# Kernel tuning notes

Hardware: AMD Instinct MI355X
Metric: run time of the kernel (lower is better)

The kernel has to match this reference:

```python
import jax, jax.numpy as jnp
import numpy as np

N = 131072          # batch of (action, condition) pairs
ACT_D = 12          # action_dim
COND_D = 256        # condition_dim
K = 256             # num_embeddings (codebook size)
E = 16              # embedding_dim
H1, H2 = 512, 256   # encoder_hidden_dims
COMMIT = 0.25       # commitment_cost
EPS_NORM = 1e-12    # F.normalize eps


def _normalize(x):
    n = jnp.linalg.norm(x, axis=-1, keepdims=True)
    return x / jnp.maximum(n, EPS_NORM)


def setup_inputs() -> dict:
    key = jax.random.key(0)
    ks = jax.random.split(key, 16)
    s = 0.02
    return {
        "actions": jax.random.normal(ks[0], (N, ACT_D), jnp.float32),
        "conditions": jax.random.normal(ks[1], (N, COND_D), jnp.float32),
        # encoder: (COND_D+ACT_D) -> H1 -> H2 -> E  (weights stored [in, out])
        "enc_w1": jax.random.normal(ks[2], (COND_D + ACT_D, H1), jnp.float32) * s,
        "enc_b1": jnp.zeros((H1,), jnp.float32),
        "enc_w2": jax.random.normal(ks[3], (H1, H2), jnp.float32) * s,
        "enc_b2": jnp.zeros((H2,), jnp.float32),
        "enc_w3": jax.random.normal(ks[4], (H2, E), jnp.float32) * s,
        "enc_b3": jnp.zeros((E,), jnp.float32),
        # decoder: (COND_D+E) -> H2 -> H1 -> ACT_D
        "dec_w1": jax.random.normal(ks[5], (COND_D + E, H2), jnp.float32) * s,
        "dec_b1": jnp.zeros((H2,), jnp.float32),
        "dec_w2": jax.random.normal(ks[6], (H2, H1), jnp.float32) * s,
        "dec_b2": jnp.zeros((H1,), jnp.float32),
        "dec_w3": jax.random.normal(ks[7], (H1, ACT_D), jnp.float32) * s,
        "dec_b3": jnp.zeros((ACT_D,), jnp.float32),
        # codebook, init U(-1/K, 1/K) like nn.Embedding in the module
        "embedding": jax.random.uniform(ks[8], (K, E), jnp.float32, -1.0 / K, 1.0 / K),
    }


def reference(actions, conditions, enc_w1, enc_b1, enc_w2, enc_b2, enc_w3, enc_b3,
              dec_w1, dec_b1, dec_w2, dec_b2, dec_w3, dec_b3, embedding):
    sg = jax.lax.stop_gradient
    elu = jax.nn.elu

    # ---- encoder ----
    x = jnp.concatenate([actions, conditions], axis=-1)          # [N, ACT_D+COND_D]
    h = elu(x @ enc_w1 + enc_b1)
    h = elu(h @ enc_w2 + enc_b2)
    z = h @ enc_w3 + enc_b3                                      # [N, E]

    # ---- vector quantizer (distance='cos') ----
    normed_in = sg(_normalize(z))                                # inputs.detach()
    normed_w = _normalize(embedding)
    distances = normed_in @ normed_w.T                           # [N, K] cosine sims

    idx = jnp.argmax(distances, axis=-1)                         # [N]
    quantized = embedding[idx]                                   # one-hot @ codebook == gather

    e_latent_loss = COMMIT * jnp.mean((sg(quantized) - z) ** 2)
    q_latent_loss = jnp.mean((quantized - sg(z)) ** 2)
    quantized_st = z + sg(quantized - z)                         # straight-through

    counts = jnp.zeros((K,), distances.dtype).at[idx].add(1.0)
    avg_probs = counts / N                                       # mean of one-hot encodings
    perplexity = jnp.exp(-jnp.sum(avg_probs * jnp.log(avg_probs + 1e-10)))

    # ---- contrastive loss (training branch, deterministic part) ----
    sortd = jnp.sort(distances, axis=0)                          # ascending per codeword
    n_pos = max(1, N // K)
    dis_pos = jnp.mean(sortd[-n_pos:, :], axis=0, keepdims=True) # [1, K] hardest positives
    dis_neg = sortd[: N // 2, :]                                 # [N//2, K]
    dis = jnp.concatenate([dis_pos, dis_neg], axis=0).T / 0.07   # [K, 1+N//2]
    # cross-entropy with target class 0
    contra_loss = jnp.mean(jax.nn.logsumexp(dis, axis=1) - dis[:, 0])

    # ---- decoder ----
    d = jnp.concatenate([quantized_st, conditions], axis=-1)     # [N, E+COND_D]
    d = elu(d @ dec_w1 + dec_b1)
    d = elu(d @ dec_w2 + dec_b2)
    reconstructed = d @ dec_w3 + dec_b3                          # [N, ACT_D]

    reconstruction_loss = jnp.mean((reconstructed - actions) ** 2)

    return (reconstructed, quantized_st, idx.astype(jnp.int32), q_latent_loss,
            e_latent_loss, contra_loss, perplexity, reconstruction_loss)
```

## Files before the change

### kernel.cpp

```cpp
#include <hip/hip_runtime.h>
#include <hip/hip_bf16.h>
#include <math.h>

#define NROWS 131072
#define ACT_D 12
#define COND_D 256
#define KEMB 256
#define EDIM 16
#define H1D 512
#define H2D 256
#define NB 16384

typedef __attribute__((ext_vector_type(8))) _Float16 half8;
typedef __attribute__((ext_vector_type(4))) float floatx4;
typedef unsigned short ushort_t;

#define LO_SCALE 4096.0f
#define INV_LO_SCALE 2.44140625e-4f


__global__ void init_kernel(int* counts, float* outScal) {
    int t = threadIdx.x;
    counts[t] = 0;
    if (t < 5) outScal[t] = 0.0f;
}

__device__ inline ushort_t f16bits(_Float16 h) { return __builtin_bit_cast(ushort_t, h); }
__device__ inline float f16pair(ushort_t a, ushort_t b) {
    return (float)__builtin_bit_cast(_Float16, a)
         + (float)__builtin_bit_cast(_Float16, b) * INV_LO_SCALE;
}
__device__ inline void splitf(float v, ushort_t& hi, ushort_t& lo) {
    _Float16 h = (_Float16)v;
    _Float16 l = (_Float16)((v - (float)h) * LO_SCALE);
    hi = f16bits(h); lo = f16bits(l);
}

__device__ inline void gload_lds16(const void* g, void* lds) {
    __builtin_amdgcn_global_load_lds((const __attribute__((address_space(1))) void*)g,
                                     (__attribute__((address_space(3))) void*)lds, 16, 0, 0);
}

__global__ __launch_bounds__(256)
void convw_kernel(const float* __restrict__ W, ushort_t* __restrict__ Whi,
                  ushort_t* __restrict__ Wlo, int K, int N, int Kp)
{
    int n = blockIdx.x;
    int k = blockIdx.y * 256 + threadIdx.x;
    if (k >= Kp) return;
    float v = (k < K) ? W[(long)k * N + n] : 0.0f;
    ushort_t h, l; splitf(v, h, l);
    Whi[(long)n * Kp + k] = h;
    Wlo[(long)n * Kp + k] = l;
}

template<int CONCAT>
__global__ __launch_bounds__(256, 3)
void gemm_f16x3_kernel(const void* A0v, const void* A1v,
                       const ushort_t* __restrict__ Bhi, const ushort_t* __restrict__ Blo,
                       const float* __restrict__ bias,
                       ushort_t* __restrict__ Chi, ushort_t* __restrict__ Clo,
                       int Nw, int Kp, int Kvalid)
{
    __shared__ uint lds[4096];
    const int tid = threadIdx.x;
    const int w = tid >> 6, l = tid & 63;
    const int quad = l >> 4, lr = l & 15;
    const long rowBase = (long)blockIdx.x * 64;
    const int colBase = blockIdx.y * 128;
    const int nQ = w * 32;

    floatx4 accH[4][2], accX[4][2];
#pragma unroll
    for (int i = 0; i < 4; ++i)
#pragma unroll
        for (int j = 0; j < 2; ++j) { accH[i][j] = (floatx4)(0.0f); accX[i][j] = (floatx4)(0.0f); }

    const long nIdx0 = colBase + nQ + lr;
    const ushort_t* pF0h = Bhi + nIdx0 * Kp + quad * 8;
    const ushort_t* pF1h = pF0h + 16 * Kp;
    const ushort_t* pF0l = Blo + nIdx0 * Kp + quad * 8;
    const ushort_t* pF1l = pF0l + 16 * Kp;

    uint4 bch0, bch1, bcl0, bcl1;
    auto loadB = [&](int k0) {
        bch0 = *(const uint4*)(pF0h + k0);
        bch1 = *(const uint4*)(pF1h + k0);
        bcl0 = *(const uint4*)(pF0l + k0);
        bcl1 = *(const uint4*)(pF1l + k0);
    };

    const ushort_t* pAh = (const ushort_t*)A0v + (rowBase + l) * Kp + w * 8;
    const ushort_t* pAl = (const ushort_t*)A1v + (rowBase + l) * Kp + w * 8;
    auto stageA0 = [&](int buf, int k0) {
        uint* d = &lds[buf * 2048 + w * 256];
        gload_lds16(pAh + k0, d);
        gload_lds16(pAl + k0, d + 1024);
    };

    const float* A1p = (const float*)A0v;
    const float* A2p = (const float*)A1v;
    const long grow = rowBase + l;

    auto aload = [&](float* v, int k0) {
        const int kk = k0 + w * 8;
        if (kk >= CONCAT && kk + 8 <= Kvalid) {
            const float* p = A2p + grow * COND_D + (kk - CONCAT);
            *(float4*)&v[0] = *(const float4*)p;
            *(float4*)&v[4] = *(const float4*)(p + 4);
        } else if (kk + 8 <= CONCAT) {
            const float* p = A1p + grow * CONCAT + kk;
            *(float4*)&v[0] = *(const float4*)p;
            *(float4*)&v[4] = *(const float4*)(p + 4);
        } else {
#pragma unroll
            for (int i = 0; i < 8; ++i) {
                int k = kk + i;
                v[i] = (k < CONCAT) ? A1p[grow * CONCAT + k]
                     : (k < Kvalid) ? A2p[grow * COND_D + (k - CONCAT)] : 0.0f;
            }
        }
    };
    auto awrite = [&](int buf, const float* v) {
        uint hh[4], ll[4];
#pragma unroll
        for (int i = 0; i < 4; ++i) {
            ushort_t h0, l0, h1, l1;
            splitf(v[2 * i], h0, l0);
            splitf(v[2 * i + 1], h1, l1);
            hh[i] = (uint)h0 | ((uint)h1 << 16);
            ll[i] = (uint)l0 | ((uint)l1 << 16);
        }
        *(uint4*)&lds[buf * 2048 + w * 256 + l * 4]        = *(uint4*)hh;
        *(uint4*)&lds[buf * 2048 + 1024 + w * 256 + l * 4] = *(uint4*)ll;
    };

    auto compute = [&](int buf) {
        const int base = buf * 2048;
        half8 bh0 = __builtin_bit_cast(half8, bch0);
        half8 bh1 = __builtin_bit_cast(half8, bch1);
        half8 bl0 = __builtin_bit_cast(half8, bcl0);
        half8 bl1 = __builtin_bit_cast(half8, bcl1);
#pragma unroll
        for (int im = 0; im < 4; ++im) {
            int aoff = base + quad * 256 + (im * 16 + lr) * 4;
            half8 ah = __builtin_bit_cast(half8, *(uint4*)&lds[aoff]);
            half8 al = __builtin_bit_cast(half8, *(uint4*)&lds[aoff + 1024]);
            accH[im][0] = __builtin_amdgcn_mfma_f32_16x16x32_f16(ah, bh0, accH[im][0], 0, 0, 0);
            accX[im][0] = __builtin_amdgcn_mfma_f32_16x16x32_f16(ah, bl0, accX[im][0], 0, 0, 0);
            accX[im][0] = __builtin_amdgcn_mfma_f32_16x16x32_f16(al, bh0, accX[im][0], 0, 0, 0);
            accH[im][1] = __builtin_amdgcn_mfma_f32_16x16x32_f16(ah, bh1, accH[im][1], 0, 0, 0);
            accX[im][1] = __builtin_amdgcn_mfma_f32_16x16x32_f16(ah, bl1, accX[im][1], 0, 0, 0);
            accX[im][1] = __builtin_amdgcn_mfma_f32_16x16x32_f16(al, bh1, accX[im][1], 0, 0, 0);
        }
    };

    const int kTiles = Kp / 32;
    int cur = 0;
    float v[8];

    if constexpr (CONCAT == 0) {
        stageA0(0, 0);
        loadB(0);
        __syncthreads();
    } else {
        aload(v, 0);
        loadB(0);
        awrite(0, v);
        __syncthreads();
    }

    for (int t = 0; t < kTiles; ++t) {
        const bool hasNext = (t + 1 < kTiles);
        const int k0n = (t + 1) * 32;
        if constexpr (CONCAT == 0) {
            if (hasNext) stageA0(cur ^ 1, k0n);
            compute(cur);
            if (hasNext) loadB(k0n);
        } else {
            if (hasNext) aload(v, k0n);
            compute(cur);
            if (hasNext) {
                awrite(cur ^ 1, v);
                loadB(k0n);
            }
        }
        __syncthreads();
        cur ^= 1;
    }

    float bv[2];
#pragma unroll
    for (int jn = 0; jn < 2; ++jn) bv[jn] = bias[colBase + nQ + jn * 16 + lr];
#pragma unroll
    for (int im = 0; im < 4; ++im) {
#pragma unroll
        for (int jn = 0; jn < 2; ++jn) {
            int n = colBase + nQ + jn * 16 + lr;
#pragma unroll
            for (int rr = 0; rr < 4; ++rr) {
                long m = rowBase + im * 16 + quad * 4 + rr;
                float x = accH[im][jn][rr] + accX[im][jn][rr] * INV_LO_SCALE + bv[jn];
                x = x > 0.0f ? x : (expf(x) - 1.0f);
                ushort_t h, lo; splitf(x, h, lo);
                long idx = m * Nw + n;
                Chi[idx] = h;
                Clo[idx] = lo;
            }
        }
    }
}

__global__ __launch_bounds__(256)
void quantize_kernel(const ushort_t* __restrict__ h2hi, const ushort_t* __restrict__ h2lo,
                     const float* __restrict__ W3,
                     const float* __restrict__ b3, const float* __restrict__ emb,
                     float* __restrict__ distT, float* __restrict__ outQ,
                     float* __restrict__ outIdx, int* __restrict__ counts,
                     float* __restrict__ qsum)
{
    __shared__ float h2t[16 * 260];
    __shared__ float w3t[16 * 260];
    __shared__ float nwt[256 * 20];
    __shared__ float zt[16 * 17];
    __shared__ float dt[16 * 257];
    __shared__ int   lcnt[256];
    __shared__ float swred[4];

    int t = threadIdx.x;
    long rowBase = (long)blockIdx.x * 16;

    for (int it = 0; it < 16; ++it) {
        long idx = (rowBase + it) * 256 + t;
        h2t[it * 260 + t] = f16pair(h2hi[idx], h2lo[idx]);
    }
    for (int it = 0; it < 16; ++it) {
        int flat = it * 256 + t;
        int j = flat >> 4, c = flat & 15;
        w3t[c * 260 + j] = W3[flat];
    }
    {
        float e0[16]; float ss = 0.f;
#pragma unroll
        for (int i = 0; i < 16; ++i) { e0[i] = emb[t * 16 + i]; ss += e0[i] * e0[i]; }
        float inv = 1.0f / fmaxf(sqrtf(ss), 1e-12f);
#pragma unroll
        for (int i = 0; i < 16; ++i) nwt[t * 20 + i] = e0[i] * inv;
    }
    lcnt[t] = 0;
    __syncthreads();

    int r = t >> 4, c = t & 15;
    float zacc = b3[c];
    for (int j4 = 0; j4 < 64; ++j4) {
        float4 h = *(const float4*)&h2t[r * 260 + j4 * 4];
        float4 w = *(const float4*)&w3t[c * 260 + j4 * 4];
        zacc += h.x * w.x + h.y * w.y + h.z * w.z + h.w * w.w;
    }
    float ss = zacc * zacc;
#pragma unroll
    for (int m = 1; m < 16; m <<= 1) ss += __shfl_xor(ss, m, 64);
    zt[r * 17 + c] = zacc / fmaxf(sqrtf(ss), 1e-12f);
    __syncthreads();

    float zr[16];
#pragma unroll
    for (int e = 0; e < 16; ++e) zr[e] = zt[r * 17 + e];
    float best = -1e30f; int bidx = 0;
    for (int cc = 0; cc < 16; ++cc) {
        int col = cc * 16 + c;
        float d = 0.f;
#pragma unroll
        for (int e4 = 0; e4 < 4; ++e4) {
            float4 wv = *(const float4*)&nwt[col * 20 + e4 * 4];
            d += zr[e4 * 4 + 0] * wv.x + zr[e4 * 4 + 1] * wv.y
               + zr[e4 * 4 + 2] * wv.z + zr[e4 * 4 + 3] * wv.w;
        }
        dt[r * 257 + col] = d;
        if (d > best || (d == best && col < bidx)) { best = d; bidx = col; }
    }
#pragma unroll
    for (int m = 1; m < 16; m <<= 1) {
        float ov = __shfl_xor(best, m, 64);
        int   oi = __shfl_xor(bidx, m, 64);
        if (ov > best || (ov == best && oi < bidx)) { best = ov; bidx = oi; }
    }

    float q = emb[bidx * 16 + c];
    outQ[(rowBase + r) * 16 + c] = q;
    float df = q - zacc;
    float part = df * df;
#pragma unroll
    for (int m = 1; m < 64; m <<= 1) part += __shfl_xor(part, m, 64);
    if ((t & 63) == 0) swred[t >> 6] = part;
    if (c == 0) {
        outIdx[rowBase + r] = (float)bidx;
        atomicAdd(&lcnt[bidx], 1);
    }
    __syncthreads();
    if (t == 0) atomicAdd(qsum, swred[0] + swred[1] + swred[2] + swred[3]);
    if (lcnt[t] > 0) atomicAdd(&counts[t], lcnt[t]);

    int rr = t & 15, cg = t >> 4;
    for (int i = 0; i < 16; ++i) {
        int col = i * 16 + cg;
        distT[(long)col * NROWS + rowBase + rr] = dt[rr * 257 + col];
    }
}

__global__ __launch_bounds__(1024)
void selA_kernel(const float* __restrict__ distT, int* __restrict__ stats)
{
    __shared__ int hist[NB];
    __shared__ int part[1024];
    int t = threadIdx.x, c = blockIdx.x;
    for (int i = t; i < NB; i += 1024) hist[i] = 0;
    __syncthreads();
    const float* col = distT + (long)c * NROWS;
    for (int i = t; i < NROWS; i += 1024) {
        float v = col[i];
        int b = (int)((v + 1.0f) * (NB * 0.5f));
        b = min(max(b, 0), NB - 1);
        atomicAdd(&hist[b], 1);
    }
    __syncthreads();
    const int CH = NB / 1024;
    int s = 0;
    for (int i = 0; i < CH; ++i) s += hist[t * CH + i];
    part[t] = s;
    __syncthreads();
    if (t == 0) {
        int target = NROWS / 2;
        int cum = 0; int chunk = 0;
        while (cum + part[chunk] < target) { cum += part[chunk]; ++chunk; }
        int b = chunk * CH;
        while (cum + hist[b] < target) { cum += hist[b]; ++b; }
        int medBin = b, needLow = target - cum, cntMed = hist[b];
        int cumA = 0; chunk = 1023;
        while (cumA + part[chunk] < 512) { cumA += part[chunk]; --chunk; }
        b = chunk * CH + CH - 1;
        while (cumA + hist[b] < 512) { cumA += hist[b]; --b; }
        int topBin = b, needTop = 512 - cumA, cntTop = hist[b];
        int* st = stats + c * 6;
        st[0] = medBin; st[1] = needLow; st[2] = cntMed;
        st[3] = topBin; st[4] = needTop; st[5] = cntTop;
    }
}

__global__ __launch_bounds__(1024)
void selB_kernel(const float* __restrict__ distT, const int* __restrict__ stats,
                 float* __restrict__ contra_sum)
{
    __shared__ float red[64];
    int t = threadIdx.x, c = blockIdx.x;
    const int* st = stats + c * 6;
    int medBin = st[0], needLow = st[1], cntMed = st[2];
    int topBin = st[3], needTop = st[4], cntTop = st[5];
    const float binw = 2.0f / NB;
    float mUp = -1.0f + (medBin + 1) * binw;
    const float INVT = 1.0f / 0.07f;
    const float* col = distT + (long)c * NROWS;
    float topS = 0.f, tbS = 0.f, lowS = 0.f, mbS = 0.f;
    for (int i = t; i < NROWS; i += 1024) {
        float v = col[i];
        int b = (int)((v + 1.0f) * (NB * 0.5f));
        b = min(max(b, 0), NB - 1);
        if (b > topBin)       topS += v;
        else if (b == topBin) tbS += v;
        if (b < medBin)       lowS += expf((v - mUp) * INVT);
        else if (b == medBin) mbS  += expf((v - mUp) * INVT);
    }
#pragma unroll
    for (int m = 1; m < 64; m <<= 1) {
        topS += __shfl_xor(topS, m, 64);
        tbS  += __shfl_xor(tbS, m, 64);
        lowS += __shfl_xor(lowS, m, 64);
        mbS  += __shfl_xor(mbS, m, 64);
    }
    if ((t & 63) == 0) {
        int wv = t >> 6;
        red[wv * 4 + 0] = topS; red[wv * 4 + 1] = tbS;
        red[wv * 4 + 2] = lowS; red[wv * 4 + 3] = mbS;
    }
    __syncthreads();
    if (t == 0) {
        float T0 = 0, T1 = 0, T2 = 0, T3 = 0;
        for (int wv = 0; wv < 16; ++wv) {
            T0 += red[wv * 4 + 0]; T1 += red[wv * 4 + 1];
            T2 += red[wv * 4 + 2]; T3 += red[wv * 4 + 3];
        }
        float dis_pos = (T0 + needTop * (T1 / cntTop)) * (1.0f / 512.0f);
        float S = T2 + needLow * (T3 / cntMed);
        float colContra = log1pf(S * expf((mUp - dis_pos) * INVT));
        atomicAdd(contra_sum, colContra);
    }
}

__global__ __launch_bounds__(256)
void dec3_kernel(const ushort_t* __restrict__ d2hi, const ushort_t* __restrict__ d2lo,
                 const float* __restrict__ W,
                 const float* __restrict__ bias, const float* __restrict__ actions,
                 float* __restrict__ rec, float* __restrict__ recon_sum)
{
    __shared__ float dtile[16 * 516];
    __shared__ float wt[512 * 12];
    __shared__ float red2[4];
    int t = threadIdx.x;
    long rowBase = (long)blockIdx.x * 16;
    for (int it = 0; it < 24; ++it) wt[it * 256 + t] = W[it * 256 + t];
    for (int it = 0; it < 32; ++it) {
        int flat = it * 256 + t;
        int r = flat >> 9, k = flat & 511;
        long idx = (rowBase + r) * 512 + k;
        dtile[r * 516 + k] = f16pair(d2hi[idx], d2lo[idx]);
    }
    __syncthreads();
    float part = 0.f;
    if (t < 192) {
        int r = t / 12, cc = t % 12;
        float acc = bias[cc];
        for (int k4 = 0; k4 < 128; ++k4) {
            float4 h = *(const float4*)&dtile[r * 516 + k4 * 4];
            acc += h.x * wt[(k4 * 4 + 0) * 12 + cc] + h.y * wt[(k4 * 4 + 1) * 12 + cc]
                 + h.z * wt[(k4 * 4 + 2) * 12 + cc] + h.w * wt[(k4 * 4 + 3) * 12 + cc];
        }
        rec[(rowBase + r) * 12 + cc] = acc;
        float df = acc - actions[(rowBase + r) * 12 + cc];
        part = df * df;
    }
#pragma unroll
    for (int m = 1; m < 64; m <<= 1) part += __shfl_xor(part, m, 64);
    if ((t & 63) == 0) red2[t >> 6] = part;
    __syncthreads();
    if (t == 0) atomicAdd(recon_sum, red2[0] + red2[1] + red2[2] + red2[3]);
}

__global__ void finalize_kernel(const int* __restrict__ counts, float* __restrict__ outScal)
{
    __shared__ float red[4];
    int t = threadIdx.x;
    float p = counts[t] * (1.0f / NROWS);
    float term = p * logf(p + 1e-10f);
#pragma unroll
    for (int m = 1; m < 64; m <<= 1) term += __shfl_xor(term, m, 64);
    if ((t & 63) == 0) red[t >> 6] = term;
    __syncthreads();
    if (t == 0) {
        float hsum = red[0] + red[1] + red[2] + red[3];
        float qsum = outScal[0], contra = outScal[2], recon = outScal[4];
        float ql = qsum * (1.0f / (NROWS * 16.0f));
        outScal[0] = ql;
        outScal[1] = 0.25f * ql;
        outScal[2] = contra * (1.0f / 256.0f);
        outScal[3] = expf(-hsum);
        outScal[4] = recon * (1.0f / (NROWS * 12.0f));
    }
}

extern "C" void kernel_launch(void* const* d_in, const int* in_sizes, int n_in,
                              void* d_out, int out_size, void* d_ws, size_t ws_size,
                              hipStream_t stream)
{
    const float* actions    = (const float*)d_in[0];
    const float* conditions = (const float*)d_in[1];
    const float* enc_w1 = (const float*)d_in[2];
    const float* enc_b1 = (const float*)d_in[3];
    const float* enc_w2 = (const float*)d_in[4];
    const float* enc_b2 = (const float*)d_in[5];
    const float* enc_w3 = (const float*)d_in[6];
    const float* enc_b3 = (const float*)d_in[7];
    const float* dec_w1 = (const float*)d_in[8];
    const float* dec_b1 = (const float*)d_in[9];
    const float* dec_w2 = (const float*)d_in[10];
    const float* dec_b2 = (const float*)d_in[11];
    const float* dec_w3 = (const float*)d_in[12];
    const float* dec_b3 = (const float*)d_in[13];
    const float* emb    = (const float*)d_in[14];

    float* out     = (float*)d_out;
    float* outRec  = out;
    float* outQ    = out + (long)NROWS * 12;
    float* outIdx  = out + (long)NROWS * 28;
    float* outScal = out + (long)NROWS * 29;

    ushort_t* wb    = (ushort_t*)d_out;
    ushort_t* w1hi  = wb;            ushort_t* w1lo  = wb + 147456;
    ushort_t* w2hi  = wb + 294912;   ushort_t* w2lo  = wb + 425984;
    ushort_t* wd1hi = wb + 557056;   ushort_t* wd1lo = wb + 630784;
    ushort_t* wd2hi = wb + 704512;   ushort_t* wd2lo = wb + 835584;

    float* ws = (float*)d_ws;
    int* counts = (int*)ws;
    int* stats  = (int*)(ws + 256);
    ushort_t* h2hi = (ushort_t*)(ws + 1792);
    ushort_t* h2lo = (ushort_t*)(ws + 16779008);
    ushort_t* d1hi = h2hi;
    ushort_t* d1lo = h2lo;
    float*    P1   = ws + 33556224;
    ushort_t* h1hi = (ushort_t*)P1;
    ushort_t* h1lo = (ushort_t*)(ws + 67110656);
    float*    distT = P1;
    ushort_t* d2hi = h1hi;
    ushort_t* d2lo = h1lo;

    hipLaunchKernelGGL(init_kernel, dim3(1), dim3(256), 0, stream, counts, outScal);
    hipLaunchKernelGGL(convw_kernel, dim3(512, 2), dim3(256), 0, stream, enc_w1, w1hi, w1lo, 268, 512, 288);
    hipLaunchKernelGGL(convw_kernel, dim3(256, 2), dim3(256), 0, stream, enc_w2, w2hi, w2lo, 512, 256, 512);
    hipLaunchKernelGGL(convw_kernel, dim3(256, 2), dim3(256), 0, stream, dec_w1, wd1hi, wd1lo, 272, 256, 288);
    hipLaunchKernelGGL(convw_kernel, dim3(512, 1), dim3(256), 0, stream, dec_w2, wd2hi, wd2lo, 256, 512, 256);
    hipLaunchKernelGGL((gemm_f16x3_kernel<ACT_D>), dim3(2048, 4), dim3(256), 0, stream,
                       (const void*)actions, (const void*)conditions, w1hi, w1lo, enc_b1,
                       h1hi, h1lo, H1D, 288, 268);
    hipLaunchKernelGGL((gemm_f16x3_kernel<0>), dim3(2048, 2), dim3(256), 0, stream,
                       (const void*)h1hi, (const void*)h1lo, w2hi, w2lo, enc_b2,
                       h2hi, h2lo, H2D, 512, 512);
    hipLaunchKernelGGL(quantize_kernel, dim3(8192), dim3(256), 0, stream,
                       h2hi, h2lo, enc_w3, enc_b3, emb, distT, outQ, outIdx, counts, &outScal[0]);
    hipLaunchKernelGGL(selA_kernel, dim3(256), dim3(1024), 0, stream, distT, stats);
    hipLaunchKernelGGL(selB_kernel, dim3(256), dim3(1024), 0, stream, distT, stats, &outScal[2]);
    hipLaunchKernelGGL((gemm_f16x3_kernel<EDIM>), dim3(2048, 2), dim3(256), 0, stream,
                       (const void*)outQ, (const void*)conditions, wd1hi, wd1lo, dec_b1,
                       d1hi, d1lo, H2D, 288, 272);
    hipLaunchKernelGGL((gemm_f16x3_kernel<0>), dim3(2048, 4), dim3(256), 0, stream,
                       (const void*)d1hi, (const void*)d1lo, wd2hi, wd2lo, dec_b2,
                       d2hi, d2lo, H1D, 256, 256);
    hipLaunchKernelGGL(dec3_kernel, dim3(8192), dim3(256), 0, stream,
                       d2hi, d2lo, dec_w3, dec_b3, actions, outRec, &outScal[4]);
    hipLaunchKernelGGL(finalize_kernel, dim3(1), dim3(256), 0, stream, counts, outScal);
}
```

Measured before the change: 1.470 ms.

## Drop LDS staging in split-f16 GEMM; load A fragments directly into registers with 2x2 warp tiling

The GEMM kernel no longer stages the A tile through shared memory with per-iteration barriers. Each wave now owns a 32x64 sub-tile in a 2x2 wave layout and loads its A and B MFMA fragments straight from global memory into registers, with register double-buffering. This removes the LDS traffic and __syncthreads, but A rows are now loaded redundantly by two waves and B columns by two waves. It also raises register pressure, which may hurt occupancy under the 3-blocks launch bound.

```diff
diff --git a/kernel.cpp b/kernel.cpp
--- a/kernel.cpp
+++ b/kernel.cpp
@@ -36,11 +36,6 @@
     hi = f16bits(h); lo = f16bits(l);
 }
 
-__device__ inline void gload_lds16(const void* g, void* lds) {
-    __builtin_amdgcn_global_load_lds((const __attribute__((address_space(1))) void*)g,
-                                     (__attribute__((address_space(3))) void*)lds, 16, 0, 0);
-}
-
 __global__ __launch_bounds__(256)
 void convw_kernel(const float* __restrict__ W, ushort_t* __restrict__ Whi,
                   ushort_t* __restrict__ Wlo, int K, int N, int Kp)
@@ -62,66 +57,79 @@
                        ushort_t* __restrict__ Chi, ushort_t* __restrict__ Clo,
                        int Nw, int Kp, int Kvalid)
 {
-    __shared__ uint lds[4096];
     const int tid = threadIdx.x;
     const int w = tid >> 6, l = tid & 63;
     const int quad = l >> 4, lr = l & 15;
+    const int wr = w & 1, wc = w >> 1;
     const long rowBase = (long)blockIdx.x * 64;
     const int colBase = blockIdx.y * 128;
-    const int nQ = w * 32;
-
-    floatx4 accH[4][2], accX[4][2];
-#pragma unroll
-    for (int i = 0; i < 4; ++i)
-#pragma unroll
-        for (int j = 0; j < 2; ++j) { accH[i][j] = (floatx4)(0.0f); accX[i][j] = (floatx4)(0.0f); }
-
-    const long nIdx0 = colBase + nQ + lr;
-    const ushort_t* pF0h = Bhi + nIdx0 * Kp + quad * 8;
-    const ushort_t* pF1h = pF0h + 16 * Kp;
-    const ushort_t* pF0l = Blo + nIdx0 * Kp + quad * 8;
-    const ushort_t* pF1l = pF0l + 16 * Kp;
-
-    uint4 bch0, bch1, bcl0, bcl1;
+
+    floatx4 accH[2][4], accX[2][4];
+#pragma unroll
+    for (int i = 0; i < 2; ++i)
+#pragma unroll
+        for (int j = 0; j < 4; ++j) { accH[i][j] = (floatx4)(0.0f); accX[i][j] = (floatx4)(0.0f); }
+
+    const long bcol = colBase + wc * 64 + lr;
+    const ushort_t* pB0h = Bhi + (bcol +  0) * (long)Kp + quad * 8;
+    const ushort_t* pB1h = Bhi + (bcol + 16) * (long)Kp + quad * 8;
+    const ushort_t* pB2h = Bhi + (bcol + 32) * (long)Kp + quad * 8;
+    const ushort_t* pB3h = Bhi + (bcol + 48) * (long)Kp + quad * 8;
+    const ushort_t* pB0l = Blo + (bcol +  0) * (long)Kp + quad * 8;
+    const ushort_t* pB1l = Blo + (bcol + 16) * (long)Kp + quad * 8;
+    const ushort_t* pB2l = Blo + (bcol + 32) * (long)Kp + quad * 8;
+    const ushort_t* pB3l = Blo + (bcol + 48) * (long)Kp + quad * 8;
+
+    uint4 b0h, b1h, b2h, b3h, b0l, b1l, b2l, b3l;
     auto loadB = [&](int k0) {
-        bch0 = *(const uint4*)(pF0h + k0);
-        bch1 = *(const uint4*)(pF1h + k0);
-        bcl0 = *(const uint4*)(pF0l + k0);
-        bcl1 = *(const uint4*)(pF1l + k0);
+        b0h = *(const uint4*)(pB0h + k0);
+        b1h = *(const uint4*)(pB1h + k0);
+        b2h = *(const uint4*)(pB2h + k0);
+        b3h = *(const uint4*)(pB3h + k0);
+        b0l = *(const uint4*)(pB0l + k0);
+        b1l = *(const uint4*)(pB1l + k0);
+        b2l = *(const uint4*)(pB2l + k0);
+        b3l = *(const uint4*)(pB3l + k0);
     };
 
-    const ushort_t* pAh = (const ushort_t*)A0v + (rowBase + l) * Kp + w * 8;
-    const ushort_t* pAl = (const ushort_t*)A1v + (rowBase + l) * Kp + w * 8;
-    auto stageA0 = [&](int buf, int k0) {
-        uint* d = &lds[buf * 2048 + w * 256];
-        gload_lds16(pAh + k0, d);
-        gload_lds16(pAl + k0, d + 1024);
+    const long arow0 = rowBase + wr * 32 + lr;
+    uint4 a0h, a1h, a0l, a1l;
+    uint4 n0h, n1h, n0l, n1l;
+    float v0[8], v1[8];
+
+    const ushort_t* pA0h = (const ushort_t*)A0v + arow0 * Kp + quad * 8;
+    const ushort_t* pA1h = pA0h + 16 * (long)Kp;
+    const ushort_t* pA0l = (const ushort_t*)A1v + arow0 * Kp + quad * 8;
+    const ushort_t* pA1l = pA0l + 16 * (long)Kp;
+    auto loadAnext = [&](int k0) {
+        n0h = *(const uint4*)(pA0h + k0);
+        n1h = *(const uint4*)(pA1h + k0);
+        n0l = *(const uint4*)(pA0l + k0);
+        n1l = *(const uint4*)(pA1l + k0);
     };
 
     const float* A1p = (const float*)A0v;
     const float* A2p = (const float*)A1v;
-    const long grow = rowBase + l;
-
-    auto aload = [&](float* v, int k0) {
-        const int kk = k0 + w * 8;
+    auto aloadRow = [&](float* v, long row, int k0) {
+        const int kk = k0 + quad * 8;
         if (kk >= CONCAT && kk + 8 <= Kvalid) {
-            const float* p = A2p + grow * COND_D + (kk - CONCAT);
+            const float* p = A2p + row * COND_D + (kk - CONCAT);
             *(float4*)&v[0] = *(const float4*)p;
             *(float4*)&v[4] = *(const float4*)(p + 4);
         } else if (kk + 8 <= CONCAT) {
-            const float* p = A1p + grow * CONCAT + kk;
+            const float* p = A1p + row * CONCAT + kk;
             *(float4*)&v[0] = *(const float4*)p;
             *(float4*)&v[4] = *(const float4*)(p + 4);
         } else {
 #pragma unroll
             for (int i = 0; i < 8; ++i) {
                 int k = kk + i;
-                v[i] = (k < CONCAT) ? A1p[grow * CONCAT + k]
-                     : (k < Kvalid) ? A2p[grow * COND_D + (k - CONCAT)] : 0.0f;
+                v[i] = (k < CONCAT) ? A1p[row * CONCAT + k]
+                     : (k < Kvalid) ? A2p[row * COND_D + (k - CONCAT)] : 0.0f;
             }
         }
     };
-    auto awrite = [&](int buf, const float* v) {
+    auto convertRow = [&](const float* v, uint4& h4, uint4& l4) {
         uint hh[4], ll[4];
 #pragma unroll
         for (int i = 0; i < 4; ++i) {
@@ -131,75 +139,92 @@
             hh[i] = (uint)h0 | ((uint)h1 << 16);
             ll[i] = (uint)l0 | ((uint)l1 << 16);
         }
-        *(uint4*)&lds[buf * 2048 + w * 256 + l * 4]        = *(uint4*)hh;
-        *(uint4*)&lds[buf * 2048 + 1024 + w * 256 + l * 4] = *(uint4*)ll;
+        h4 = *(uint4*)hh; l4 = *(uint4*)ll;
     };
 
-    auto compute = [&](int buf) {
-        const int base = buf * 2048;
-        half8 bh0 = __builtin_bit_cast(half8, bch0);
-        half8 bh1 = __builtin_bit_cast(half8, bch1);
-        half8 bl0 = __builtin_bit_cast(half8, bcl0);
-        half8 bl1 = __builtin_bit_cast(half8, bcl1);
-#pragma unroll
-        for (int im = 0; im < 4; ++im) {
-            int aoff = base + quad * 256 + (im * 16 + lr) * 4;
-            half8 ah = __builtin_bit_cast(half8, *(uint4*)&lds[aoff]);
-            half8 al = __builtin_bit_cast(half8, *(uint4*)&lds[aoff + 1024]);
-            accH[im][0] = __builtin_amdgcn_mfma_f32_16x16x32_f16(ah, bh0, accH[im][0], 0, 0, 0);
-            accX[im][0] = __builtin_amdgcn_mfma_f32_16x16x32_f16(ah, bl0, accX[im][0], 0, 0, 0);
-            accX[im][0] = __builtin_amdgcn_mfma_f32_16x16x32_f16(al, bh0, accX[im][0], 0, 0, 0);
-            accH[im][1] = __builtin_amdgcn_mfma_f32_16x16x32_f16(ah, bh1, accH[im][1], 0, 0, 0);
-            accX[im][1] = __builtin_amdgcn_mfma_f32_16x16x32_f16(ah, bl1, accX[im][1], 0, 0, 0);
-            accX[im][1] = __builtin_amdgcn_mfma_f32_16x16x32_f16(al, bh1, accX[im][1], 0, 0, 0);
-        }
+    auto compute = [&]() {
+        half8 A0h = __builtin_bit_cast(half8, a0h), A0l = __builtin_bit_cast(half8, a0l);
+        half8 A1h = __builtin_bit_cast(half8, a1h), A1l = __builtin_bit_cast(half8, a1l);
+        half8 B0h = __builtin_bit_cast(half8, b0h), B0l = __builtin_bit_cast(half8, b0l);
+        half8 B1h = __builtin_bit_cast(half8, b1h), B1l = __builtin_bit_cast(half8, b1l);
+        half8 B2h = __builtin_bit_cast(half8, b2h), B2l = __builtin_bit_cast(half8, b2l);
+        half8 B3h = __builtin_bit_cast(half8, b3h), B3l = __builtin_bit_cast(half8, b3l);
+        accH[0][0] = __builtin_amdgcn_mfma_f32_16x16x32_f16(A0h, B0h, accH[0][0], 0, 0, 0);
+        accX[0][0] = __builtin_amdgcn_mfma_f32_16x16x32_f16(A0h, B0l, accX[0][0], 0, 0, 0);
+        accX[0][0] = __builtin_amdgcn_mfma_f32_16x16x32_f16(A0l, B0h, accX[0][0], 0, 0, 0);
+        accH[0][1] = __builtin_amdgcn_mfma_f32_16x16x32_f16(A0h, B1h, accH[0][1], 0, 0, 0);
+        accX[0][1] = __builtin_amdgcn_mfma_f32_16x16x32_f16(A0h, B1l, accX[0][1], 0, 0, 0);
+        accX[0][1] = __builtin_amdgcn_mfma_f32_16x16x32_f16(A0l, B1h, accX[0][1], 0, 0, 0);
+        accH[0][2] = __builtin_amdgcn_mfma_f32_16x16x32_f16(A0h, B2h, accH[0][2], 0, 0, 0);
+        accX[0][2] = __builtin_amdgcn_mfma_f32_16x16x32_f16(A0h, B2l, accX[0][2], 0, 0, 0);
+        accX[0][2] = __builtin_amdgcn_mfma_f32_16x16x32_f16(A0l, B2h, accX[0][2], 0, 0, 0);
+        accH[0][3] = __builtin_amdgcn_mfma_f32_16x16x32_f16(A0h, B3h, accH[0][3], 0, 0, 0);
+        accX[0][3] = __builtin_amdgcn_mfma_f32_16x16x32_f16(A0h, B3l, accX[0][3], 0, 0, 0);
+        accX[0][3] = __builtin_amdgcn_mfma_f32_16x16x32_f16(A0l, B3h, accX[0][3], 0, 0, 0);
+        accH[1][0] = __builtin_amdgcn_mfma_f32_16x16x32_f16(A1h, B0h, accH[1][0], 0, 0, 0);
+        accX[1][0] = __builtin_amdgcn_mfma_f32_16x16x32_f16(A1h, B0l, accX[1][0], 0, 0, 0);
+        accX[1][0] = __builtin_amdgcn_mfma_f32_16x16x32_f16(A1l, B0h, accX[1][0], 0, 0, 0);
+        accH[1][1] = __builtin_amdgcn_mfma_f32_16x16x32_f16(A1h, B1h, accH[1][1], 0, 0, 0);
+        accX[1][1] = __builtin_amdgcn_mfma_f32_16x16x32_f16(A1h, B1l, accX[1][1], 0, 0, 0);
+        accX[1][1] = __builtin_amdgcn_mfma_f32_16x16x32_f16(A1l, B1h, accX[1][1], 0, 0, 0);
+        accH[1][2] = __builtin_amdgcn_mfma_f32_16x16x32_f16(A1h, B2h, accH[1][2], 0, 0, 0);
+        accX[1][2] = __builtin_amdgcn_mfma_f32_16x16x32_f16(A1h, B2l, accX[1][2], 0, 0, 0);
+        accX[1][2] = __builtin_amdgcn_mfma_f32_16x16x32_f16(A1l, B2h, accX[1][2], 0, 0, 0);
+        accH[1][3] = __builtin_amdgcn_mfma_f32_16x16x32_f16(A1h, B3h, accH[1][3], 0, 0, 0);
+        accX[1][3] = __builtin_amdgcn_mfma_f32_16x16x32_f16(A1h, B3l, accX[1][3], 0, 0, 0);
+        accX[1][3] = __builtin_amdgcn_mfma_f32_16x16x32_f16(A1l, B3h, accX[1][3], 0, 0, 0);
     };
 
     const int kTiles = Kp / 32;
-    int cur = 0;
-    float v[8];
 
     if constexpr (CONCAT == 0) {
-        stageA0(0, 0);
+        n0h = *(const uint4*)(pA0h); n1h = *(const uint4*)(pA1h);
+        n0l = *(const uint4*)(pA0l); n1l = *(const uint4*)(pA1l);
         loadB(0);
-        __syncthreads();
+        a0h = n0h; a1h = n1h; a0l = n0l; a1l = n1l;
+        for (int t = 0; t < kTiles; ++t) {
+            const bool hn = (t + 1 < kTiles);
+            const int k0n = (t + 1) * 32;
+            if (hn) loadAnext(k0n);
+            compute();
+            if (hn) {
+                loadB(k0n);
+                a0h = n0h; a1h = n1h; a0l = n0l; a1l = n1l;
+            }
+        }
     } else {
-        aload(v, 0);
+        aloadRow(v0, arow0, 0);
+        aloadRow(v1, arow0 + 16, 0);
         loadB(0);
-        awrite(0, v);
-        __syncthreads();
-    }
-
-    for (int t = 0; t < kTiles; ++t) {
-        const bool hasNext = (t + 1 < kTiles);
-        const int k0n = (t + 1) * 32;
-        if constexpr (CONCAT == 0) {
-            if (hasNext) stageA0(cur ^ 1, k0n);
-            compute(cur);
-            if (hasNext) loadB(k0n);
-        } else {
-            if (hasNext) aload(v, k0n);
-            compute(cur);
-            if (hasNext) {
-                awrite(cur ^ 1, v);
+        convertRow(v0, a0h, a0l);
+        convertRow(v1, a1h, a1l);
+        for (int t = 0; t < kTiles; ++t) {
+            const bool hn = (t + 1 < kTiles);
+            const int k0n = (t + 1) * 32;
+            if (hn) {
+                aloadRow(v0, arow0, k0n);
+                aloadRow(v1, arow0 + 16, k0n);
+            }
+            compute();
+            if (hn) {
                 loadB(k0n);
+                convertRow(v0, a0h, a0l);
+                convertRow(v1, a1h, a1l);
             }
         }
-        __syncthreads();
-        cur ^= 1;
-    }
-
-    float bv[2];
-#pragma unroll
-    for (int jn = 0; jn < 2; ++jn) bv[jn] = bias[colBase + nQ + jn * 16 + lr];
-#pragma unroll
-    for (int im = 0; im < 4; ++im) {
-#pragma unroll
-        for (int jn = 0; jn < 2; ++jn) {
-            int n = colBase + nQ + jn * 16 + lr;
+    }
+
+    float bv[4];
+#pragma unroll
+    for (int jn = 0; jn < 4; ++jn) bv[jn] = bias[colBase + wc * 64 + jn * 16 + lr];
+#pragma unroll
+    for (int im = 0; im < 2; ++im) {
+#pragma unroll
+        for (int jn = 0; jn < 4; ++jn) {
+            int n = colBase + wc * 64 + jn * 16 + lr;
 #pragma unroll
             for (int rr = 0; rr < 4; ++rr) {
-                long m = rowBase + im * 16 + quad * 4 + rr;
+                long m = rowBase + wr * 32 + im * 16 + quad * 4 + rr;
                 float x = accH[im][jn][rr] + accX[im][jn][rr] * INV_LO_SCALE + bv[jn];
                 x = x > 0.0f ? x : (expf(x) - 1.0f);
                 ushort_t h, lo; splitf(x, h, lo);
```

Measured after the change: 2.023 ms. 37.6% more time.
